# Kernel optimization log

Measured on AMD Instinct MI355X. Metric: run time of the kernel, lower is better.

Reference implementation:

```python
import jax, jax.numpy as jnp
import numpy as np

GAMMA = 1.0
ALPHA = 0.5
EMBED_DIM = 256
N = 8192
M = 8192


def setup_inputs() -> dict:
    key = jax.random.key(0)
    k1, k2, k3, k4 = jax.random.split(key, 4)
    a = jax.random.normal(k1, (N, EMBED_DIM), dtype=jnp.float32)
    b = jax.random.normal(k2, (M, EMBED_DIM), dtype=jnp.float32)
    # torch.nn.Linear default init: U(-1/sqrt(fan_in), 1/sqrt(fan_in))
    lim = 1.0 / np.sqrt(EMBED_DIM)
    Wq = jax.random.uniform(k3, (EMBED_DIM, EMBED_DIM), jnp.float32, -lim, lim)
    Wk = jax.random.uniform(k4, (EMBED_DIM, EMBED_DIM), jnp.float32, -lim, lim)
    return {"a": a, "b": b, "Wq": Wq, "Wk": Wk}


def reference(a, b, Wq, Wk):
    # Vectorized Gram matrix of HybridKernelMethod.forward over all (a_i, b_j) pairs.
    inv_sqrt_d = np.float32(1.0 / np.sqrt(EMBED_DIM))
    ab = a @ b.T                                           # [N, M] cross dot products
    # RBF part: ||a_i - b_j||^2 = ||a_i||^2 + ||b_j||^2 - 2 a_i.b_j
    sq = (jnp.sum(a * a, axis=-1)[:, None]
          + jnp.sum(b * b, axis=-1)[None, :] - 2.0 * ab)
    rbf_sim = jnp.exp(-GAMMA * sq)                         # [N, M]
    # Attention part: per pair, q k^T is a 1x1 matrix, so softmax == 1 exactly.
    q = a @ Wq.T                                           # [N, D]
    k = b @ Wk.T                                           # [M, D]
    s = (q @ k.T) * inv_sqrt_d                             # [N, M] scores
    scores = jax.nn.softmax(s[..., None], axis=-1)[..., 0]  # all-ones, faithful to 1x1 softmax
    attn_sim = scores * ab                                 # sum((scores @ v) * x) == scores * (a.b)
    return (1.0 - ALPHA) * rbf_sim + ALPHA * attn_sim      # [N, M] Gram matrix
```

## Files before the change

### kernel.cpp

```cpp
#include <hip/hip_runtime.h>
#include <stdint.h>

#define DIM 256
#define NROWS 8192
#define OUTC 8192

#define BM 128
#define BN 128
#define BK 64

typedef __bf16 bf16x8_t __attribute__((ext_vector_type(8)));
typedef float f32x4_t __attribute__((ext_vector_type(4)));

__device__ __forceinline__ unsigned short f2bf_rne(float f) {
    unsigned int u = __float_as_uint(f);
    u += 0x7FFFu + ((u >> 16) & 1u);
    return (unsigned short)(u >> 16);
}

__global__ void prep_kernel(const float* __restrict__ src,
                            unsigned short* __restrict__ dst,
                            float* __restrict__ norms) {
    const int w = threadIdx.x >> 6;
    const int l = threadIdx.x & 63;
    const int row = blockIdx.x * 4 + w;
    const float4 v = reinterpret_cast<const float4*>(src + (size_t)row * DIM)[l];
    float ss = v.x * v.x + v.y * v.y + v.z * v.z + v.w * v.w;
#pragma unroll
    for (int off = 32; off > 0; off >>= 1) ss += __shfl_down(ss, off);
    if (l == 0) norms[row] = ss;
    ushort4 o = make_ushort4(f2bf_rne(v.x), f2bf_rne(v.y), f2bf_rne(v.z), f2bf_rne(v.w));
    reinterpret_cast<ushort4*>(dst + (size_t)row * DIM)[l] = o;
}

__global__ __launch_bounds__(256) void gemm_kernel(
        const unsigned short* __restrict__ aB,
        const unsigned short* __restrict__ bB,
        const float* __restrict__ na,
        const float* __restrict__ nb,
        float* __restrict__ out) {
    __shared__ unsigned short sA[BM * BK];
    __shared__ unsigned short sB[BN * BK];

    const int t = threadIdx.x;
    const int w = t >> 6;
    const int l = t & 63;
    const int wr = w >> 1;
    const int wc = w & 1;

    const int by = blockIdx.x >> 6;
    const int bx = blockIdx.x & 63;
    const int row0 = by * BM;
    const int col0 = bx * BN;

    f32x4_t acc[4][4];
#pragma unroll
    for (int m = 0; m < 4; ++m)
#pragma unroll
        for (int n = 0; n < 4; ++n) acc[m][n] = (f32x4_t)0.0f;

    const int lr = l >> 3;
    const int lc = (l & 7) * 8;
    const int fr = l & 15;
    const int kq = l >> 4;

#pragma unroll
    for (int kt = 0; kt < DIM / BK; ++kt) {
#pragma unroll
        for (int it = 0; it < 4; ++it) {
            const int rg = w * 4 + it;
            const int r = rg * 8 + lr;
            const unsigned short* ga = aB + (size_t)(row0 + r) * DIM + kt * BK + lc;
            const unsigned short* gb = bB + (size_t)(col0 + r) * DIM + kt * BK + lc;
            __builtin_amdgcn_global_load_lds(
                (const __attribute__((address_space(1))) void*)ga,
                (__attribute__((address_space(3))) void*)&sA[rg * 8 * BK], 16, 0, 0);
            __builtin_amdgcn_global_load_lds(
                (const __attribute__((address_space(1))) void*)gb,
                (__attribute__((address_space(3))) void*)&sB[rg * 8 * BK], 16, 0, 0);
        }
        __syncthreads();

#pragma unroll
        for (int ks = 0; ks < 2; ++ks) {
            bf16x8_t af[4], bfr[4];
#pragma unroll
            for (int m = 0; m < 4; ++m)
                af[m] = *reinterpret_cast<const bf16x8_t*>(
                    &sA[(wr * 64 + m * 16 + fr) * BK + ks * 32 + kq * 8]);
#pragma unroll
            for (int n = 0; n < 4; ++n)
                bfr[n] = *reinterpret_cast<const bf16x8_t*>(
                    &sB[(wc * 64 + n * 16 + fr) * BK + ks * 32 + kq * 8]);
#pragma unroll
            for (int m = 0; m < 4; ++m)
#pragma unroll
                for (int n = 0; n < 4; ++n)
                    acc[m][n] = __builtin_amdgcn_mfma_f32_16x16x32_bf16(
                        af[m], bfr[n], acc[m][n], 0, 0, 0);
        }
        __syncthreads();
    }

#pragma unroll
    for (int m = 0; m < 4; ++m) {
        const int rbase = row0 + wr * 64 + m * 16 + kq * 4;
#pragma unroll
        for (int q = 0; q < 4; ++q) {
            const int r = rbase + q;
            const float nar = na[r];
            const size_t ro = (size_t)r * OUTC;
#pragma unroll
            for (int n = 0; n < 4; ++n) {
                const int c = col0 + wc * 64 + n * 16 + fr;
                const float dot = acc[m][n][q];
                const float sq = nar + nb[c] - 2.0f * dot;
                out[ro + c] = 0.5f * __expf(-sq) + 0.5f * dot;
            }
        }
    }
}

__global__ void naive_kernel(const float* __restrict__ a,
                             const float* __restrict__ b,
                             float* __restrict__ out) {
    const size_t idx = (size_t)blockIdx.x * 256 + threadIdx.x;
    const int i = (int)(idx >> 13);
    const int j = (int)(idx & 8191);
    float dot = 0.f, naa = 0.f, nbb = 0.f;
    for (int k = 0; k < DIM; ++k) {
        const float x = a[(size_t)i * DIM + k];
        const float y = b[(size_t)j * DIM + k];
        dot += x * y; naa += x * x; nbb += y * y;
    }
    const float sq = naa + nbb - 2.0f * dot;
    out[idx] = 0.5f * __expf(-sq) + 0.5f * dot;
}

extern "C" void kernel_launch(void* const* d_in, const int* in_sizes, int n_in,
                              void* d_out, int out_size, void* d_ws, size_t ws_size,
                              hipStream_t stream) {
    const float* a = (const float*)d_in[0];
    const float* b = (const float*)d_in[1];
    float* out = (float*)d_out;

    const size_t bf_bytes = (size_t)NROWS * DIM * sizeof(unsigned short);
    const size_t nrm_bytes = (size_t)NROWS * sizeof(float);
    const size_t need = 2 * bf_bytes + 2 * nrm_bytes;

    if (ws_size >= need) {
        unsigned short* aBf = (unsigned short*)d_ws;
        unsigned short* bBf = (unsigned short*)((char*)d_ws + bf_bytes);
        float* na = (float*)((char*)d_ws + 2 * bf_bytes);
        float* nb = (float*)((char*)d_ws + 2 * bf_bytes + nrm_bytes);

        prep_kernel<<<NROWS / 4, 256, 0, stream>>>(a, aBf, na);
        prep_kernel<<<NROWS / 4, 256, 0, stream>>>(b, bBf, nb);
        gemm_kernel<<<(NROWS / BM) * (NROWS / BN), 256, 0, stream>>>(aBf, bBf, na, nb, out);
    } else {
        naive_kernel<<<((size_t)NROWS * NROWS) / 256, 256, 0, stream>>>(a, b, out);
    }
}
```

Before: 88.93 us.

## Persistent double-buffered GEMM with swizzled LDS, 32x32 MFMA, deferred stores

```diff
diff --git a/kernel.cpp b/kernel.cpp
--- a/kernel.cpp
+++ b/kernel.cpp
@@ -2,15 +2,19 @@
 #include <stdint.h>
 
 #define DIM 256
-#define NROWS 8192
-#define OUTC 8192
-
+#define NR 8192
 #define BM 128
 #define BN 128
 #define BK 64
-
-typedef __bf16 bf16x8_t __attribute__((ext_vector_type(8)));
-typedef float f32x4_t __attribute__((ext_vector_type(4)));
+#define TPB 8
+#define GRID 512
+
+typedef __bf16 bf16x8 __attribute__((ext_vector_type(8)));
+typedef float  f32x16 __attribute__((ext_vector_type(16)));
+typedef float  f32x4  __attribute__((ext_vector_type(4)));
+
+#define MEMFENCE asm volatile("" ::: "memory")
+#define WAITV(N) asm volatile("s_waitcnt vmcnt(" #N ")" ::: "memory")
 
 __device__ __forceinline__ unsigned short f2bf_rne(float f) {
     unsigned int u = __float_as_uint(f);
@@ -18,106 +22,206 @@
     return (unsigned short)(u >> 16);
 }
 
-__global__ void prep_kernel(const float* __restrict__ src,
-                            unsigned short* __restrict__ dst,
-                            float* __restrict__ norms) {
+__global__ void prep_kernel(const float* __restrict__ a,
+                            const float* __restrict__ b,
+                            unsigned short* __restrict__ aB,
+                            unsigned short* __restrict__ bB,
+                            float* __restrict__ na,
+                            float* __restrict__ nb) {
     const int w = threadIdx.x >> 6;
     const int l = threadIdx.x & 63;
-    const int row = blockIdx.x * 4 + w;
+    const int blk = blockIdx.x;
+    const float* src; unsigned short* dst; float* nrm; int row;
+    if (blk < 2048) { src = a; dst = aB; nrm = na; row = blk * 4 + w; }
+    else            { src = b; dst = bB; nrm = nb; row = (blk - 2048) * 4 + w; }
     const float4 v = reinterpret_cast<const float4*>(src + (size_t)row * DIM)[l];
     float ss = v.x * v.x + v.y * v.y + v.z * v.z + v.w * v.w;
 #pragma unroll
     for (int off = 32; off > 0; off >>= 1) ss += __shfl_down(ss, off);
-    if (l == 0) norms[row] = ss;
+    if (l == 0) nrm[row] = ss;
     ushort4 o = make_ushort4(f2bf_rne(v.x), f2bf_rne(v.y), f2bf_rne(v.z), f2bf_rne(v.w));
     reinterpret_cast<ushort4*>(dst + (size_t)row * DIM)[l] = o;
 }
 
-__global__ __launch_bounds__(256) void gemm_kernel(
+#define STAGE(row0_, kt_, buf_)                                                   \
+    do {                                                                          \
+        _Pragma("unroll")                                                         \
+        for (int it_ = 0; it_ < 4; ++it_) {                                       \
+            __builtin_amdgcn_global_load_lds(                                     \
+                (const __attribute__((address_space(1))) void*)(aB +              \
+                    (size_t)((row0_) + rowIt[it_]) * DIM + (kt_) * BK + colIt[it_]), \
+                (__attribute__((address_space(3))) void*)&sA[buf_][(w * 4 + it_) * 512], \
+                16, 0, 0);                                                        \
+        }                                                                         \
+        _Pragma("unroll")                                                         \
+        for (int it_ = 0; it_ < 4; ++it_) {                                       \
+            __builtin_amdgcn_global_load_lds(                                     \
+                (const __attribute__((address_space(1))) void*)(bB +              \
+                    (size_t)(col0 + rowIt[it_]) * DIM + (kt_) * BK + colIt[it_]), \
+                (__attribute__((address_space(3))) void*)&sB[buf_][(w * 4 + it_) * 512], \
+                16, 0, 0);                                                        \
+        }                                                                         \
+    } while (0)
+
+#define COMPUTE(buf_)                                                             \
+    do {                                                                          \
+        _Pragma("unroll")                                                         \
+        for (int ks_ = 0; ks_ < 4; ++ks_) {                                       \
+            bf16x8 af[2], bfv[2];                                                 \
+            _Pragma("unroll")                                                     \
+            for (int mi_ = 0; mi_ < 2; ++mi_)                                     \
+                af[mi_] = *(const bf16x8*)((const char*)&sA[buf_][0] +            \
+                    baseA[mi_] + ((XA[mi_] ^ (ks_ << 1)) << 4));                  \
+            _Pragma("unroll")                                                     \
+            for (int ni_ = 0; ni_ < 2; ++ni_)                                     \
+                bfv[ni_] = *(const bf16x8*)((const char*)&sB[buf_][0] +           \
+                    baseB[ni_] + ((XB[ni_] ^ (ks_ << 1)) << 4));                  \
+            _Pragma("unroll")                                                     \
+            for (int mi_ = 0; mi_ < 2; ++mi_)                                     \
+                _Pragma("unroll")                                                 \
+                for (int ni_ = 0; ni_ < 2; ++ni_)                                 \
+                    acc[mi_][ni_] = __builtin_amdgcn_mfma_f32_32x32x16_bf16(      \
+                        af[mi_], bfv[ni_], acc[mi_][ni_], 0, 0, 0);               \
+        }                                                                         \
+    } while (0)
+
+__global__ __launch_bounds__(256, 2) void gemm_kernel(
         const unsigned short* __restrict__ aB,
         const unsigned short* __restrict__ bB,
         const float* __restrict__ na,
         const float* __restrict__ nb,
         float* __restrict__ out) {
-    __shared__ unsigned short sA[BM * BK];
-    __shared__ unsigned short sB[BN * BK];
+    __shared__ unsigned short sA[2][8192];
+    __shared__ unsigned short sB[2][8192];
 
     const int t = threadIdx.x;
-    const int w = t >> 6;
-    const int l = t & 63;
-    const int wr = w >> 1;
-    const int wc = w & 1;
-
-    const int by = blockIdx.x >> 6;
-    const int bx = blockIdx.x & 63;
-    const int row0 = by * BM;
+    const int w = t >> 6, l = t & 63;
+    const int wr = w >> 1, wc = w & 1;
+    const int hi = l >> 5, lr = l & 31;
+
+    const int bx = (int)blockIdx.x & 63;
+    const int bb = (int)blockIdx.x >> 6;
     const int col0 = bx * BN;
 
-    f32x4_t acc[4][4];
-#pragma unroll
-    for (int m = 0; m < 4; ++m)
-#pragma unroll
-        for (int n = 0; n < 4; ++n) acc[m][n] = (f32x4_t)0.0f;
-
-    const int lr = l >> 3;
-    const int lc = (l & 7) * 8;
-    const int fr = l & 15;
-    const int kq = l >> 4;
-
-#pragma unroll
-    for (int kt = 0; kt < DIM / BK; ++kt) {
-#pragma unroll
-        for (int it = 0; it < 4; ++it) {
-            const int rg = w * 4 + it;
-            const int r = rg * 8 + lr;
-            const unsigned short* ga = aB + (size_t)(row0 + r) * DIM + kt * BK + lc;
-            const unsigned short* gb = bB + (size_t)(col0 + r) * DIM + kt * BK + lc;
-            __builtin_amdgcn_global_load_lds(
-                (const __attribute__((address_space(1))) void*)ga,
-                (__attribute__((address_space(3))) void*)&sA[rg * 8 * BK], 16, 0, 0);
-            __builtin_amdgcn_global_load_lds(
-                (const __attribute__((address_space(1))) void*)gb,
-                (__attribute__((address_space(3))) void*)&sB[rg * 8 * BK], 16, 0, 0);
+    int rowIt[4], colIt[4];
+#pragma unroll
+    for (int it = 0; it < 4; ++it) {
+        int G = (w * 4 + it) * 64 + l;
+        int rp = G >> 4, pos = G & 15;
+        int c2 = pos ^ (rp & 15);
+        rowIt[it] = 2 * rp + (c2 >> 3);
+        colIt[it] = (c2 & 7) * 8;
+    }
+    int baseA[2], XA[2], baseB[2], XB[2];
+#pragma unroll
+    for (int mi = 0; mi < 2; ++mi) {
+        int r = wr * 64 + mi * 32 + lr;
+        baseA[mi] = (r >> 1) * 256;
+        XA[mi] = (((r & 1) * 8) | hi) ^ ((r >> 1) & 15);
+        int rb = wc * 64 + mi * 32 + lr;
+        baseB[mi] = (rb >> 1) * 256;
+        XB[mi] = (((rb & 1) * 8) | hi) ^ ((rb >> 1) & 15);
+    }
+
+    float nbv[2];
+#pragma unroll
+    for (int ni = 0; ni < 2; ++ni) nbv[ni] = nb[col0 + wc * 64 + ni * 32 + lr];
+
+    float outB[2][16];
+    f32x4 nav[2][4];
+
+    {
+        const int r0 = bb * BM;
+        STAGE(r0, 0, 0);
+        STAGE(r0, 1, 1);
+    }
+    MEMFENCE;
+
+    for (int ti = 0; ti < TPB; ++ti) {
+        const int row0 = (bb + ti * 8) * BM;
+        f32x16 acc[2][2];
+#pragma unroll
+        for (int mi = 0; mi < 2; ++mi)
+#pragma unroll
+            for (int ni = 0; ni < 2; ++ni) acc[mi][ni] = (f32x16)0.0f;
+
+        if (ti == 0) { WAITV(0); } else { WAITV(32); }
+        __builtin_amdgcn_s_barrier(); MEMFENCE;
+        COMPUTE(0);
+        MEMFENCE; __builtin_amdgcn_s_barrier(); MEMFENCE;
+        STAGE(row0, 2, 0);
+        MEMFENCE;
+        if (ti > 0) {
+            const int prow = row0 - 1024 + wr * 64 + 32 + 4 * hi;
+            const int pcol = col0 + wc * 64 + lr;
+#pragma unroll
+            for (int ni = 0; ni < 2; ++ni)
+#pragma unroll
+                for (int tt = 0; tt < 16; ++tt) {
+                    int q = tt & 3, p = tt >> 2;
+                    __builtin_nontemporal_store(outB[ni][tt],
+                        &out[(size_t)(prow + 8 * p + q) * 8192 + pcol + ni * 32]);
+                }
         }
-        __syncthreads();
-
-#pragma unroll
-        for (int ks = 0; ks < 2; ++ks) {
-            bf16x8_t af[4], bfr[4];
-#pragma unroll
-            for (int m = 0; m < 4; ++m)
-                af[m] = *reinterpret_cast<const bf16x8_t*>(
-                    &sA[(wr * 64 + m * 16 + fr) * BK + ks * 32 + kq * 8]);
-#pragma unroll
-            for (int n = 0; n < 4; ++n)
-                bfr[n] = *reinterpret_cast<const bf16x8_t*>(
-                    &sB[(wc * 64 + n * 16 + fr) * BK + ks * 32 + kq * 8]);
-#pragma unroll
-            for (int m = 0; m < 4; ++m)
-#pragma unroll
-                for (int n = 0; n < 4; ++n)
-                    acc[m][n] = __builtin_amdgcn_mfma_f32_16x16x32_bf16(
-                        af[m], bfr[n], acc[m][n], 0, 0, 0);
-        }
-        __syncthreads();
-    }
-
-#pragma unroll
-    for (int m = 0; m < 4; ++m) {
-        const int rbase = row0 + wr * 64 + m * 16 + kq * 4;
-#pragma unroll
-        for (int q = 0; q < 4; ++q) {
-            const int r = rbase + q;
-            const float nar = na[r];
-            const size_t ro = (size_t)r * OUTC;
-#pragma unroll
-            for (int n = 0; n < 4; ++n) {
-                const int c = col0 + wc * 64 + n * 16 + fr;
-                const float dot = acc[m][n][q];
-                const float sq = nar + nb[c] - 2.0f * dot;
-                out[ro + c] = 0.5f * __expf(-sq) + 0.5f * dot;
+        MEMFENCE;
+
+        __builtin_amdgcn_s_barrier(); MEMFENCE;
+        COMPUTE(1);
+        MEMFENCE; __builtin_amdgcn_s_barrier(); MEMFENCE;
+        STAGE(row0, 3, 1);
+        MEMFENCE;
+
+        if (ti == 0) { WAITV(8); } else { WAITV(40); }
+        __builtin_amdgcn_s_barrier(); MEMFENCE;
+        COMPUTE(0);
+        MEMFENCE; __builtin_amdgcn_s_barrier(); MEMFENCE;
+#pragma unroll
+        for (int mi = 0; mi < 2; ++mi)
+#pragma unroll
+            for (int p = 0; p < 4; ++p)
+                nav[mi][p] = *(const f32x4*)&na[row0 + wr * 64 + mi * 32 + 8 * p + 4 * hi];
+        MEMFENCE;
+        if (ti < TPB - 1) STAGE(row0 + 1024, 0, 0);
+        MEMFENCE;
+
+        if (ti == TPB - 1) { WAITV(8); } else { WAITV(16); }
+        __builtin_amdgcn_s_barrier(); MEMFENCE;
+        COMPUTE(1);
+        MEMFENCE; __builtin_amdgcn_s_barrier(); MEMFENCE;
+        if (ti < TPB - 1) STAGE(row0 + 1024, 1, 1);
+        MEMFENCE;
+
+#pragma unroll
+        for (int mi = 0; mi < 2; ++mi)
+#pragma unroll
+            for (int ni = 0; ni < 2; ++ni)
+#pragma unroll
+                for (int tt = 0; tt < 16; ++tt) {
+                    int q = tt & 3, p = tt >> 2;
+                    int row = row0 + wr * 64 + mi * 32 + 8 * p + 4 * hi + q;
+                    int col = col0 + wc * 64 + ni * 32 + lr;
+                    float dot = acc[mi][ni][tt];
+                    float sq = nav[mi][p][q] + nbv[ni] - 2.0f * dot;
+                    float v = 0.5f * __expf(-sq) + 0.5f * dot;
+                    if (mi == 0)
+                        __builtin_nontemporal_store(v, &out[(size_t)row * 8192 + col]);
+                    else
+                        outB[ni][tt] = v;
+                }
+        MEMFENCE;
+    }
+
+    {
+        const int prow = (bb + 56) * BM + wr * 64 + 32 + 4 * hi;
+        const int pcol = col0 + wc * 64 + lr;
+#pragma unroll
+        for (int ni = 0; ni < 2; ++ni)
+#pragma unroll
+            for (int tt = 0; tt < 16; ++tt) {
+                int q = tt & 3, p = tt >> 2;
+                __builtin_nontemporal_store(outB[ni][tt],
+                    &out[(size_t)(prow + 8 * p + q) * 8192 + pcol + ni * 32]);
             }
-        }
     }
 }
 
@@ -144,8 +248,8 @@
     const float* b = (const float*)d_in[1];
     float* out = (float*)d_out;
 
-    const size_t bf_bytes = (size_t)NROWS * DIM * sizeof(unsigned short);
-    const size_t nrm_bytes = (size_t)NROWS * sizeof(float);
+    const size_t bf_bytes = (size_t)NR * DIM * sizeof(unsigned short);
+    const size_t nrm_bytes = (size_t)NR * sizeof(float);
     const size_t need = 2 * bf_bytes + 2 * nrm_bytes;
 
     if (ws_size >= need) {
@@ -154,10 +258,9 @@
         float* na = (float*)((char*)d_ws + 2 * bf_bytes);
         float* nb = (float*)((char*)d_ws + 2 * bf_bytes + nrm_bytes);
 
-        prep_kernel<<<NROWS / 4, 256, 0, stream>>>(a, aBf, na);
-        prep_kernel<<<NROWS / 4, 256, 0, stream>>>(b, bBf, nb);
-        gemm_kernel<<<(NROWS / BM) * (NROWS / BN), 256, 0, stream>>>(aBf, bBf, na, nb, out);
+        prep_kernel<<<4096, 256, 0, stream>>>(a, b, aBf, bBf, na, nb);
+        gemm_kernel<<<GRID, 256, 0, stream>>>(aBf, bBf, na, nb, out);
     } else {
-        naive_kernel<<<((size_t)NROWS * NROWS) / 256, 256, 0, stream>>>(a, b, out);
-    }
-}
+        naive_kernel<<<((size_t)NR * NR) / 256, 256, 0, stream>>>(a, b, out);
+    }
+}
```

Measured after the change: 77.17 us. -13.2%, faster.
